# Kernel tuning notes

Measured on AMD Instinct MI355X. Metric: run time of the kernel, lower is better.

Reference implementation:

```python
import jax, jax.numpy as jnp
import numpy as np


def setup_inputs() -> dict:
    key = jax.random.key(0)
    k0, k1, k2 = jax.random.split(key, 3)
    B, S, H, D = 2, 2048, 16, 128  # flash-attn layout [batch, seq, heads, head_dim]
    q = jax.random.normal(k0, (B, S, H, D), dtype=jnp.float32)
    k = jax.random.normal(k1, (B, S, H, D), dtype=jnp.float32)
    v = jax.random.normal(k2, (B, S, H, D), dtype=jnp.float32)
    return {"_in0": q, "_in1": k, "_in2": v}


def reference(_in0, _in1, _in2):
    # Ring attention computes exact (non-causal, default) scaled dot-product
    # attention over the full sequence; the ring KV rotation is a distributed
    # execution detail, not a change in math. Single-device math:
    q, k, v = _in0, _in1, _in2
    D = q.shape[-1]
    scale = 1.0 / jnp.sqrt(jnp.asarray(D, dtype=q.dtype))
    # scores: [B, H, Sq, Sk]
    scores = jnp.einsum("bqhd,bkhd->bhqk", q, k) * scale
    probs = jax.nn.softmax(scores, axis=-1)
    out = jnp.einsum("bhqk,bkhd->bqhd", probs, v)
    return out
```

## Files before the change

kernel.cpp:

```cpp
#include <hip/hip_runtime.h>
#include <hip/hip_bf16.h>

typedef __attribute__((ext_vector_type(8))) short short8;
typedef __attribute__((ext_vector_type(16))) float f32x16;
typedef __attribute__((ext_vector_type(4))) unsigned int uint4v;

#define NB 2
#define NS 2048
#define NH 16
#define ND 128
#define ROWS (NH * ND)
#define KVBLK 64
#define QBLK 128
#define NTILE (NS / KVBLK)
#define NQB (NS / QBLK)
#define TILEB 16384

__device__ __forceinline__ unsigned short f2bf(float f) {
  union { __hip_bfloat16 b; unsigned short u; } c;
  c.b = __float2bfloat16(f);
  return c.u;
}

__device__ __forceinline__ short8 pack8(float4 a, float4 b, float s) {
  short8 r;
  r[0] = (short)f2bf(a.x * s); r[1] = (short)f2bf(a.y * s);
  r[2] = (short)f2bf(a.z * s); r[3] = (short)f2bf(a.w * s);
  r[4] = (short)f2bf(b.x * s); r[5] = (short)f2bf(b.y * s);
  r[6] = (short)f2bf(b.z * s); r[7] = (short)f2bf(b.w * s);
  return r;
}

__device__ __forceinline__ void dma16(const void* g, void* l) {
  __builtin_amdgcn_global_load_lds(
      (const __attribute__((address_space(1))) unsigned int*)g,
      (__attribute__((address_space(3))) unsigned int*)l, 16, 0, 0);
}

__device__ __forceinline__ void pl32swap(unsigned int& a, unsigned int& b) {
  asm("v_permlane32_swap_b32 %0, %1" : "+v"(a), "+v"(b));
}

__global__ __launch_bounds__(256) void prepass_kv(
    const float* __restrict__ Kg, const float* __restrict__ Vg,
    char* __restrict__ Kbt, char* __restrict__ Vbt) {
  const int blk = blockIdx.x;
  const int t = blk & (NTILE - 1);
  const int bh = blk >> 5;
  const int h = bh & (NH - 1);
  const int b = bh >> 4;
  const int tid = threadIdx.x;

  const size_t ibase = (size_t)b * NS * ROWS + (size_t)h * ND + (size_t)t * KVBLK * ROWS;
  const float* Kp = Kg + ibase;
  const float* Vp = Vg + ibase;
  char* Kt = Kbt + (size_t)blk * TILEB;
  char* Vt = Vbt + (size_t)blk * TILEB;

#pragma unroll
  for (int j = 0; j < 4; ++j) {
    const int r = j * 16 + (tid >> 4);
    const int c = tid & 15;
    const float* src = Kp + (size_t)r * ROWS + c * 8;
    float4 a = *reinterpret_cast<const float4*>(src);
    float4 d = *reinterpret_cast<const float4*>(src + 4);
    *reinterpret_cast<short8*>(Kt + r * 256 + (((c ^ (r & 15)) << 4))) = pack8(a, d, 1.0f);
  }

  __shared__ float vt[64][129];
#pragma unroll
  for (int j = 0; j < 4; ++j) {
    const int r = j * 16 + (tid >> 4);
    const int c0 = (tid & 15) * 8;
    float4 a = *reinterpret_cast<const float4*>(Vp + (size_t)r * ROWS + c0);
    float4 d = *reinterpret_cast<const float4*>(Vp + (size_t)r * ROWS + c0 + 4);
    vt[r][c0 + 0] = a.x; vt[r][c0 + 1] = a.y; vt[r][c0 + 2] = a.z; vt[r][c0 + 3] = a.w;
    vt[r][c0 + 4] = d.x; vt[r][c0 + 5] = d.y; vt[r][c0 + 6] = d.z; vt[r][c0 + 7] = d.w;
  }
  __syncthreads();
#pragma unroll
  for (int it = 0; it < 4; ++it) {
    const int item = it * 256 + tid;
    const int r = item >> 4;
    const int j = item & 15;
    const int d = 2 * r + (j >> 3);
    const int k0 = (j & 7) * 8;
    short8 o8;
#pragma unroll
    for (int i = 0; i < 8; ++i) o8[i] = (short)f2bf(vt[k0 + i][d]);
    *reinterpret_cast<short8*>(Vt + r * 256 + (((j ^ (r & 15)) << 4))) = o8;
  }
}

__global__ __launch_bounds__(256, 2) void fattn_fwd(
    const float* __restrict__ Qg, const char* __restrict__ Kbt,
    const char* __restrict__ Vbt, float* __restrict__ Og) {
  __shared__ __align__(16) char lds[65536];
  const int tid = threadIdx.x;
  const int l = tid & 63;
  const int w = tid >> 6;
  const int l31 = l & 31;
  const int hi2 = l >> 5;

  const int orig = blockIdx.x;
  const int wg = (orig & 7) * 64 + (orig >> 3);
  const int qblk = wg & (NQB - 1);
  const int bh = wg >> 4;
  const int h = bh & (NH - 1);
  const int b = bh >> 4;

  const float* Qp = Qg + (size_t)b * NS * ROWS + (size_t)h * ND;
  float* Op = Og + (size_t)b * NS * ROWS + (size_t)h * ND;
  const char* Ktiles = Kbt + (size_t)bh * NTILE * TILEB;
  const char* Vtiles = Vbt + (size_t)bh * NTILE * TILEB;

  const float scale = 0.08838834764831845f * 1.4426950408889634f;

  const int qrow = qblk * QBLK + w * 32 + l31;
  short8 qf[8];
  {
    const float* qr = Qp + (size_t)qrow * ROWS + hi2 * 8;
#pragma unroll
    for (int ks = 0; ks < 8; ++ks) {
      float4 a = *reinterpret_cast<const float4*>(qr + ks * 16);
      float4 c = *reinterpret_cast<const float4*>(qr + ks * 16 + 4);
      qf[ks] = pack8(a, c, scale);
    }
  }

  auto stage = [&](int t, char* kd, char* vd) {
    const char* Ksrc = Ktiles + (size_t)t * TILEB;
    const char* Vsrc = Vtiles + (size_t)t * TILEB;
#pragma unroll
    for (int i = 0; i < 4; ++i) {
      const int instr = w * 4 + i;
      dma16(Ksrc + instr * 1024 + l * 16, kd + instr * 1024);
    }
#pragma unroll
    for (int i = 0; i < 4; ++i) {
      const int instr = w * 4 + i;
      dma16(Vsrc + instr * 1024 + l * 16, vd + instr * 1024);
    }
  };

  f32x16 o[4];
#pragma unroll
  for (int dt = 0; dt < 4; ++dt) o[dt] = 0.f;
  float l_acc = 0.f;

  stage(0, lds, lds + 16384);
  asm volatile("s_waitcnt vmcnt(0)" ::: "memory");
  __syncthreads();

#pragma unroll 1
  for (int t = 0; t < NTILE; ++t) {
    char* ksb = lds + (t & 1) * 32768;
    char* vtb = ksb + 16384;
    if (t + 1 < NTILE) {
      char* kn = lds + ((t + 1) & 1) * 32768;
      stage(t + 1, kn, kn + 16384);
    }

    short8 pf[4];
#pragma unroll
    for (int mt = 0; mt < 2; ++mt) {
      f32x16 acc = 0.f;
      const int row = mt * 32 + l31;
      const int rsw = (row & 15) << 4;
      __builtin_amdgcn_s_setprio(1);
#pragma unroll
      for (int ks = 0; ks < 8; ++ks) {
        short8 kf = *reinterpret_cast<const short8*>(
            ksb + row * 256 + ((ks * 32 + hi2 * 16) ^ rsw));
        acc = __builtin_amdgcn_mfma_f32_32x32x16_bf16(kf, qf[ks], acc, 0, 0, 0);
      }
      __builtin_amdgcn_s_setprio(0);
      f32x16 p;
#pragma unroll
      for (int r = 0; r < 16; ++r) p[r] = exp2f(acc[r]);
      {
        float s = 0.f;
#pragma unroll
        for (int r = 0; r < 16; ++r) s += p[r];
        l_acc += s;
      }
#pragma unroll
      for (int half = 0; half < 2; ++half) {
        unsigned int X[4];
#pragma unroll
        for (int j = 0; j < 4; ++j)
          X[j] = (unsigned int)f2bf(p[half * 8 + 2 * j]) |
                 ((unsigned int)f2bf(p[half * 8 + 2 * j + 1]) << 16);
        pl32swap(X[0], X[2]);
        pl32swap(X[1], X[3]);
        uint4v u = {X[0], X[1], X[2], X[3]};
        pf[mt * 2 + half] = __builtin_bit_cast(short8, u);
      }
    }

    __builtin_amdgcn_s_setprio(1);
#pragma unroll
    for (int dt = 0; dt < 4; ++dt) {
      const int d = dt * 32 + l31;
      const int vrow = d >> 1;
      const int vsw = (vrow & 15) << 4;
      const int doff = (d & 1) * 128;
#pragma unroll
      for (int ks = 0; ks < 4; ++ks) {
        short8 vf = *reinterpret_cast<const short8*>(
            vtb + vrow * 256 + ((doff + ks * 32 + hi2 * 16) ^ vsw));
        o[dt] = __builtin_amdgcn_mfma_f32_32x32x16_bf16(vf, pf[ks], o[dt], 0, 0, 0);
      }
    }
    __builtin_amdgcn_s_setprio(0);

    if (t + 1 < NTILE) {
      asm volatile("s_waitcnt vmcnt(0)" ::: "memory");
      __syncthreads();
    }
  }

  const float lt = l_acc + __shfl_xor(l_acc, 32);
  const float inv = 1.0f / lt;
  float* orow = Op + (size_t)qrow * ROWS;
#pragma unroll
  for (int dt = 0; dt < 4; ++dt) {
#pragma unroll
    for (int g = 0; g < 4; ++g) {
      float4 v;
      v.x = o[dt][g * 4 + 0] * inv;
      v.y = o[dt][g * 4 + 1] * inv;
      v.z = o[dt][g * 4 + 2] * inv;
      v.w = o[dt][g * 4 + 3] * inv;
      *reinterpret_cast<float4*>(orow + dt * 32 + g * 8 + hi2 * 4) = v;
    }
  }
}

extern "C" void kernel_launch(void* const* d_in, const int* in_sizes, int n_in,
                              void* d_out, int out_size, void* d_ws, size_t ws_size,
                              hipStream_t stream) {
  const float* q = (const float*)d_in[0];
  const float* k = (const float*)d_in[1];
  const float* v = (const float*)d_in[2];
  float* out = (float*)d_out;
  (void)in_sizes; (void)n_in; (void)out_size; (void)ws_size;
  char* Kbt = (char*)d_ws;
  char* Vbt = Kbt + (size_t)NB * NH * NTILE * TILEB;
  prepass_kv<<<dim3(NB * NH * NTILE), dim3(256), 0, stream>>>(k, v, Kbt, Vbt);
  fattn_fwd<<<dim3(NQB * NB * NH), dim3(256), 0, stream>>>(q, Kbt, Vbt, out);
}
```

Before: 110.5 us.

## Double Q block per workgroup and process two KV tiles per sync window

Query block size grows from 128 to 256 rows with 512 threads (8 waves), so each staged K/V tile is reused by twice as many query rows. LDS doubles to 128KB to hold two KV tiles per double-buffered window, which halves the number of barriers. The QK step now interleaves four independent MFMA accumulators for more ILP, and per-lane LDS offsets are computed once up front. The risks are register pressure under the new launch bounds, which could cause spills, and only one workgroup fitting per CU.

```diff
diff --git a/kernel.cpp b/kernel.cpp
--- a/kernel.cpp
+++ b/kernel.cpp
@@ -11,9 +11,10 @@
 #define ND 128
 #define ROWS (NH * ND)
 #define KVBLK 64
-#define QBLK 128
+#define QBLK 256
 #define NTILE (NS / KVBLK)
 #define NQB (NS / QBLK)
+#define NWIN (NTILE / 2)
 #define TILEB 16384
 
 __device__ __forceinline__ unsigned short f2bf(float f) {
@@ -92,10 +93,10 @@
   }
 }
 
-__global__ __launch_bounds__(256, 2) void fattn_fwd(
+__global__ __launch_bounds__(512, 2) void fattn_fwd(
     const float* __restrict__ Qg, const char* __restrict__ Kbt,
     const char* __restrict__ Vbt, float* __restrict__ Og) {
-  __shared__ __align__(16) char lds[65536];
+  __shared__ __align__(16) char lds[131072];
   const int tid = threadIdx.x;
   const int l = tid & 63;
   const int w = tid >> 6;
@@ -103,9 +104,9 @@
   const int hi2 = l >> 5;
 
   const int orig = blockIdx.x;
-  const int wg = (orig & 7) * 64 + (orig >> 3);
+  const int wg = (orig & 7) * 32 + (orig >> 3);
   const int qblk = wg & (NQB - 1);
-  const int bh = wg >> 4;
+  const int bh = wg >> 3;
   const int h = bh & (NH - 1);
   const int b = bh >> 4;
 
@@ -128,18 +129,29 @@
     }
   }
 
-  auto stage = [&](int t, char* kd, char* vd) {
-    const char* Ksrc = Ktiles + (size_t)t * TILEB;
-    const char* Vsrc = Vtiles + (size_t)t * TILEB;
-#pragma unroll
-    for (int i = 0; i < 4; ++i) {
-      const int instr = w * 4 + i;
-      dma16(Ksrc + instr * 1024 + l * 16, kd + instr * 1024);
-    }
-#pragma unroll
-    for (int i = 0; i < 4; ++i) {
-      const int instr = w * 4 + i;
-      dma16(Vsrc + instr * 1024 + l * 16, vd + instr * 1024);
+  int qkoff[8], pvoff[4];
+  {
+    const int rsw = (l31 & 15) << 4;
+#pragma unroll
+    for (int ks = 0; ks < 8; ++ks)
+      qkoff[ks] = l31 * 256 + ((ks * 32 + hi2 * 16) ^ rsw);
+    const int vsw = ((l31 >> 1) & 15) << 4;
+#pragma unroll
+    for (int ks = 0; ks < 4; ++ks)
+      pvoff[ks] = (l31 >> 1) * 256 +
+                  ((((l31 & 1) * 128) + ks * 32 + hi2 * 16) ^ vsw);
+  }
+
+  auto stageT = [&](int t, int s) {
+    const char* Ks = Ktiles + (size_t)t * TILEB;
+    const char* Vs = Vtiles + (size_t)t * TILEB;
+    char* kd = lds + s * 32768;
+    char* vd = kd + 16384;
+#pragma unroll
+    for (int i = 0; i < 2; ++i) {
+      const int off = i * 8192 + w * 1024;
+      dma16(Ks + off + l * 16, kd + off);
+      dma16(Vs + off + l * 16, vd + off);
     }
   };
 
@@ -148,73 +160,80 @@
   for (int dt = 0; dt < 4; ++dt) o[dt] = 0.f;
   float l_acc = 0.f;
 
-  stage(0, lds, lds + 16384);
+  auto smpack = [&](const f32x16& acc, short8* out2) {
+    f32x16 p;
+#pragma unroll
+    for (int r = 0; r < 16; ++r) p[r] = exp2f(acc[r]);
+    float s = 0.f;
+#pragma unroll
+    for (int r = 0; r < 16; ++r) s += p[r];
+    l_acc += s;
+#pragma unroll
+    for (int half = 0; half < 2; ++half) {
+      unsigned int X[4];
+#pragma unroll
+      for (int j = 0; j < 4; ++j)
+        X[j] = (unsigned int)f2bf(p[half * 8 + 2 * j]) |
+               ((unsigned int)f2bf(p[half * 8 + 2 * j + 1]) << 16);
+      pl32swap(X[0], X[2]);
+      pl32swap(X[1], X[3]);
+      uint4v u = {X[0], X[1], X[2], X[3]};
+      out2[half] = __builtin_bit_cast(short8, u);
+    }
+  };
+
+  auto pv = [&](const char* vb, const short8* pf) {
+    __builtin_amdgcn_s_setprio(1);
+#pragma unroll
+    for (int dt = 0; dt < 4; ++dt) {
+#pragma unroll
+      for (int ks = 0; ks < 4; ++ks) {
+        short8 vf = *reinterpret_cast<const short8*>(vb + pvoff[ks] + dt * 4096);
+        o[dt] = __builtin_amdgcn_mfma_f32_32x32x16_bf16(vf, pf[ks], o[dt], 0, 0, 0);
+      }
+    }
+    __builtin_amdgcn_s_setprio(0);
+  };
+
+  stageT(0, 0);
+  stageT(1, 1);
   asm volatile("s_waitcnt vmcnt(0)" ::: "memory");
   __syncthreads();
 
 #pragma unroll 1
-  for (int t = 0; t < NTILE; ++t) {
-    char* ksb = lds + (t & 1) * 32768;
-    char* vtb = ksb + 16384;
-    if (t + 1 < NTILE) {
-      char* kn = lds + ((t + 1) & 1) * 32768;
-      stage(t + 1, kn, kn + 16384);
-    }
+  for (int j = 0; j < NWIN; ++j) {
+    if (j + 1 < NWIN) {
+      const int s0 = ((j & 1) ^ 1) * 2;
+      stageT(2 * j + 2, s0);
+      stageT(2 * j + 3, s0 + 1);
+    }
+    const char* kb0 = lds + (j & 1) * 65536;
+    const char* kb1 = kb0 + 32768;
+
+    f32x16 a00 = 0.f, a01 = 0.f, a10 = 0.f, a11 = 0.f;
+    __builtin_amdgcn_s_setprio(1);
+#pragma unroll
+    for (int ks = 0; ks < 8; ++ks) {
+      short8 k0 = *reinterpret_cast<const short8*>(kb0 + qkoff[ks]);
+      a00 = __builtin_amdgcn_mfma_f32_32x32x16_bf16(k0, qf[ks], a00, 0, 0, 0);
+      short8 k1 = *reinterpret_cast<const short8*>(kb0 + qkoff[ks] + 8192);
+      a01 = __builtin_amdgcn_mfma_f32_32x32x16_bf16(k1, qf[ks], a01, 0, 0, 0);
+      short8 k2 = *reinterpret_cast<const short8*>(kb1 + qkoff[ks]);
+      a10 = __builtin_amdgcn_mfma_f32_32x32x16_bf16(k2, qf[ks], a10, 0, 0, 0);
+      short8 k3 = *reinterpret_cast<const short8*>(kb1 + qkoff[ks] + 8192);
+      a11 = __builtin_amdgcn_mfma_f32_32x32x16_bf16(k3, qf[ks], a11, 0, 0, 0);
+    }
+    __builtin_amdgcn_s_setprio(0);
 
     short8 pf[4];
-#pragma unroll
-    for (int mt = 0; mt < 2; ++mt) {
-      f32x16 acc = 0.f;
-      const int row = mt * 32 + l31;
-      const int rsw = (row & 15) << 4;
-      __builtin_amdgcn_s_setprio(1);
-#pragma unroll
-      for (int ks = 0; ks < 8; ++ks) {
-        short8 kf = *reinterpret_cast<const short8*>(
-            ksb + row * 256 + ((ks * 32 + hi2 * 16) ^ rsw));
-        acc = __builtin_amdgcn_mfma_f32_32x32x16_bf16(kf, qf[ks], acc, 0, 0, 0);
-      }
-      __builtin_amdgcn_s_setprio(0);
-      f32x16 p;
-#pragma unroll
-      for (int r = 0; r < 16; ++r) p[r] = exp2f(acc[r]);
-      {
-        float s = 0.f;
-#pragma unroll
-        for (int r = 0; r < 16; ++r) s += p[r];
-        l_acc += s;
-      }
-#pragma unroll
-      for (int half = 0; half < 2; ++half) {
-        unsigned int X[4];
-#pragma unroll
-        for (int j = 0; j < 4; ++j)
-          X[j] = (unsigned int)f2bf(p[half * 8 + 2 * j]) |
-                 ((unsigned int)f2bf(p[half * 8 + 2 * j + 1]) << 16);
-        pl32swap(X[0], X[2]);
-        pl32swap(X[1], X[3]);
-        uint4v u = {X[0], X[1], X[2], X[3]};
-        pf[mt * 2 + half] = __builtin_bit_cast(short8, u);
-      }
-    }
-
-    __builtin_amdgcn_s_setprio(1);
-#pragma unroll
-    for (int dt = 0; dt < 4; ++dt) {
-      const int d = dt * 32 + l31;
-      const int vrow = d >> 1;
-      const int vsw = (vrow & 15) << 4;
-      const int doff = (d & 1) * 128;
-#pragma unroll
-      for (int ks = 0; ks < 4; ++ks) {
-        short8 vf = *reinterpret_cast<const short8*>(
-            vtb + vrow * 256 + ((doff + ks * 32 + hi2 * 16) ^ vsw));
-        o[dt] = __builtin_amdgcn_mfma_f32_32x32x16_bf16(vf, pf[ks], o[dt], 0, 0, 0);
-      }
-    }
-    __builtin_amdgcn_s_setprio(0);
-
-    if (t + 1 < NTILE) {
+    smpack(a00, pf + 0);
+    smpack(a01, pf + 2);
+    pv(kb0 + 16384, pf);
+    smpack(a10, pf + 0);
+    smpack(a11, pf + 2);
+    pv(kb1 + 16384, pf);
+
+    if (j + 1 < NWIN) {
       asm volatile("s_waitcnt vmcnt(0)" ::: "memory");
       __syncthreads();
     }
@@ -248,5 +267,5 @@
   char* Kbt = (char*)d_ws;
   char* Vbt = Kbt + (size_t)NB * NH * NTILE * TILEB;
   prepass_kv<<<dim3(NB * NH * NTILE), dim3(256), 0, stream>>>(k, v, Kbt, Vbt);
-  fattn_fwd<<<dim3(NQB * NB * NH), dim3(256), 0, stream>>>(q, Kbt, Vbt, out);
-}
+  fattn_fwd<<<dim3(NQB * NB * NH), dim3(512), 0, stream>>>(q, Kbt, Vbt, out);
+}
```

New measurement: 110.8 us. No clear change (+0.3%).

## Split KV across two workgroups, double Q rows per wave, add combine pass

Applied to the files above, without the earlier changes.

Each wave now handles 64 query rows, so every K/V fragment read from LDS feeds two MFMAs. The KV sequence is split in two halves processed by separate workgroups, which keeps the grid size unchanged. A separate combine kernel sums the partial outputs and normalizers. The prepass writes K/V directly in MFMA fragment order, so the swizzled address math goes away. The cost is extra global traffic for the fp32 partial outputs (two full-size buffers), a third kernel launch, and higher register pressure from 8 accumulators per wave.

```diff
diff --git a/kernel.cpp b/kernel.cpp
--- a/kernel.cpp
+++ b/kernel.cpp
@@ -11,10 +11,14 @@
 #define ND 128
 #define ROWS (NH * ND)
 #define KVBLK 64
-#define QBLK 128
 #define NTILE (NS / KVBLK)
+#define QBLK 256
 #define NQB (NS / QBLK)
+#define NSPLIT 2
+#define TPS (NTILE / NSPLIT)
 #define TILEB 16384
+#define ELEMS ((size_t)NB * NH * NS * ND)
+#define LCNT ((size_t)NB * NS * NH)
 
 __device__ __forceinline__ unsigned short f2bf(float f) {
   union { __hip_bfloat16 b; unsigned short u; } c;
@@ -43,58 +47,77 @@
 
 __global__ __launch_bounds__(256) void prepass_kv(
     const float* __restrict__ Kg, const float* __restrict__ Vg,
-    char* __restrict__ Kbt, char* __restrict__ Vbt) {
+    char* __restrict__ Kimg, char* __restrict__ Vimg) {
   const int blk = blockIdx.x;
   const int t = blk & (NTILE - 1);
   const int bh = blk >> 5;
   const int h = bh & (NH - 1);
   const int b = bh >> 4;
   const int tid = threadIdx.x;
+  const int l = tid & 63;
+  const int l31 = l & 31;
+  const int hi2 = l >> 5;
 
   const size_t ibase = (size_t)b * NS * ROWS + (size_t)h * ND + (size_t)t * KVBLK * ROWS;
   const float* Kp = Kg + ibase;
   const float* Vp = Vg + ibase;
-  char* Kt = Kbt + (size_t)blk * TILEB;
-  char* Vt = Vbt + (size_t)blk * TILEB;
+  char* Kt = Kimg + (size_t)blk * TILEB;
+  char* Vt = Vimg + (size_t)blk * TILEB;
+
+  __shared__ float st[64][129];
 
 #pragma unroll
   for (int j = 0; j < 4; ++j) {
     const int r = j * 16 + (tid >> 4);
-    const int c = tid & 15;
-    const float* src = Kp + (size_t)r * ROWS + c * 8;
-    float4 a = *reinterpret_cast<const float4*>(src);
-    float4 d = *reinterpret_cast<const float4*>(src + 4);
-    *reinterpret_cast<short8*>(Kt + r * 256 + (((c ^ (r & 15)) << 4))) = pack8(a, d, 1.0f);
-  }
-
-  __shared__ float vt[64][129];
+    const int c0 = (tid & 15) * 8;
+    float4 a = *reinterpret_cast<const float4*>(Kp + (size_t)r * ROWS + c0);
+    float4 d = *reinterpret_cast<const float4*>(Kp + (size_t)r * ROWS + c0 + 4);
+    st[r][c0 + 0] = a.x; st[r][c0 + 1] = a.y; st[r][c0 + 2] = a.z; st[r][c0 + 3] = a.w;
+    st[r][c0 + 4] = d.x; st[r][c0 + 5] = d.y; st[r][c0 + 6] = d.z; st[r][c0 + 7] = d.w;
+  }
+  __syncthreads();
+#pragma unroll
+  for (int it = 0; it < 4; ++it) {
+    const int item = it * 256 + tid;
+    const int g = item >> 6;
+    const int ll = item & 63;
+    const int row = (g >> 3) * 32 + (ll & 31);
+    const int kc = (g & 7) * 16 + (ll >> 5) * 8;
+    short8 o8;
+#pragma unroll
+    for (int e = 0; e < 8; ++e) o8[e] = (short)f2bf(st[row][kc + e]);
+    *reinterpret_cast<short8*>(Kt + (g * 64 + ll) * 16) = o8;
+  }
+  __syncthreads();
+
 #pragma unroll
   for (int j = 0; j < 4; ++j) {
     const int r = j * 16 + (tid >> 4);
     const int c0 = (tid & 15) * 8;
     float4 a = *reinterpret_cast<const float4*>(Vp + (size_t)r * ROWS + c0);
     float4 d = *reinterpret_cast<const float4*>(Vp + (size_t)r * ROWS + c0 + 4);
-    vt[r][c0 + 0] = a.x; vt[r][c0 + 1] = a.y; vt[r][c0 + 2] = a.z; vt[r][c0 + 3] = a.w;
-    vt[r][c0 + 4] = d.x; vt[r][c0 + 5] = d.y; vt[r][c0 + 6] = d.z; vt[r][c0 + 7] = d.w;
+    st[r][c0 + 0] = a.x; st[r][c0 + 1] = a.y; st[r][c0 + 2] = a.z; st[r][c0 + 3] = a.w;
+    st[r][c0 + 4] = d.x; st[r][c0 + 5] = d.y; st[r][c0 + 6] = d.z; st[r][c0 + 7] = d.w;
   }
   __syncthreads();
 #pragma unroll
   for (int it = 0; it < 4; ++it) {
     const int item = it * 256 + tid;
-    const int r = item >> 4;
-    const int j = item & 15;
-    const int d = 2 * r + (j >> 3);
-    const int k0 = (j & 7) * 8;
+    const int g = item >> 6;
+    const int ll = item & 63;
+    const int d = (g >> 2) * 32 + (ll & 31);
+    const int kv = (g & 3) * 16 + (ll >> 5) * 8;
     short8 o8;
 #pragma unroll
-    for (int i = 0; i < 8; ++i) o8[i] = (short)f2bf(vt[k0 + i][d]);
-    *reinterpret_cast<short8*>(Vt + r * 256 + (((j ^ (r & 15)) << 4))) = o8;
-  }
-}
-
-__global__ __launch_bounds__(256, 2) void fattn_fwd(
-    const float* __restrict__ Qg, const char* __restrict__ Kbt,
-    const char* __restrict__ Vbt, float* __restrict__ Og) {
+    for (int e = 0; e < 8; ++e) o8[e] = (short)f2bf(st[kv + e][d]);
+    *reinterpret_cast<short8*>(Vt + (g * 64 + ll) * 16) = o8;
+  }
+}
+
+__global__ __launch_bounds__(256, 2) void fattn_split(
+    const float* __restrict__ Qg, const char* __restrict__ Kimg,
+    const char* __restrict__ Vimg, float* __restrict__ Obase,
+    float* __restrict__ Lbase) {
   __shared__ __align__(16) char lds[65536];
   const int tid = threadIdx.x;
   const int l = tid & 63;
@@ -105,135 +128,165 @@
   const int orig = blockIdx.x;
   const int wg = (orig & 7) * 64 + (orig >> 3);
   const int qblk = wg & (NQB - 1);
+  const int split = (wg >> 3) & 1;
   const int bh = wg >> 4;
   const int h = bh & (NH - 1);
   const int b = bh >> 4;
 
+  float* Opart = Obase + (size_t)split * ELEMS;
+  float* Lpart = Lbase + (size_t)split * LCNT;
+
   const float* Qp = Qg + (size_t)b * NS * ROWS + (size_t)h * ND;
-  float* Op = Og + (size_t)b * NS * ROWS + (size_t)h * ND;
-  const char* Ktiles = Kbt + (size_t)bh * NTILE * TILEB;
-  const char* Vtiles = Vbt + (size_t)bh * NTILE * TILEB;
+  const char* Kt = Kimg + (size_t)bh * NTILE * TILEB;
+  const char* Vt = Vimg + (size_t)bh * NTILE * TILEB;
 
   const float scale = 0.08838834764831845f * 1.4426950408889634f;
 
-  const int qrow = qblk * QBLK + w * 32 + l31;
-  short8 qf[8];
+  const int qrow0 = qblk * QBLK + w * 64 + l31;
+  short8 qf0[8], qf1[8];
   {
-    const float* qr = Qp + (size_t)qrow * ROWS + hi2 * 8;
+    const float* qr0 = Qp + (size_t)qrow0 * ROWS + hi2 * 8;
+    const float* qr1 = qr0 + (size_t)32 * ROWS;
 #pragma unroll
     for (int ks = 0; ks < 8; ++ks) {
-      float4 a = *reinterpret_cast<const float4*>(qr + ks * 16);
-      float4 c = *reinterpret_cast<const float4*>(qr + ks * 16 + 4);
-      qf[ks] = pack8(a, c, scale);
-    }
-  }
-
-  auto stage = [&](int t, char* kd, char* vd) {
-    const char* Ksrc = Ktiles + (size_t)t * TILEB;
-    const char* Vsrc = Vtiles + (size_t)t * TILEB;
+      float4 a = *reinterpret_cast<const float4*>(qr0 + ks * 16);
+      float4 c = *reinterpret_cast<const float4*>(qr0 + ks * 16 + 4);
+      qf0[ks] = pack8(a, c, scale);
+      float4 d = *reinterpret_cast<const float4*>(qr1 + ks * 16);
+      float4 e = *reinterpret_cast<const float4*>(qr1 + ks * 16 + 4);
+      qf1[ks] = pack8(d, e, scale);
+    }
+  }
+
+  const int lo16 = l * 16;
+
+  auto stage = [&](int t, int slot) {
+    const char* Ks = Kt + (size_t)t * TILEB;
+    const char* Vs = Vt + (size_t)t * TILEB;
+    char* kd = lds + slot * 32768;
+    char* vd = kd + 16384;
 #pragma unroll
     for (int i = 0; i < 4; ++i) {
-      const int instr = w * 4 + i;
-      dma16(Ksrc + instr * 1024 + l * 16, kd + instr * 1024);
-    }
-#pragma unroll
-    for (int i = 0; i < 4; ++i) {
-      const int instr = w * 4 + i;
-      dma16(Vsrc + instr * 1024 + l * 16, vd + instr * 1024);
+      const int off = (w * 4 + i) * 1024;
+      dma16(Ks + off + lo16, kd + off);
+      dma16(Vs + off + lo16, vd + off);
     }
   };
 
-  f32x16 o[4];
-#pragma unroll
-  for (int dt = 0; dt < 4; ++dt) o[dt] = 0.f;
-  float l_acc = 0.f;
-
-  stage(0, lds, lds + 16384);
+  f32x16 o[4][2];
+#pragma unroll
+  for (int dt = 0; dt < 4; ++dt) {
+    o[dt][0] = 0.f;
+    o[dt][1] = 0.f;
+  }
+  float lac0 = 0.f, lac1 = 0.f;
+
+  auto sm = [&](const f32x16& acc, short8& f0, short8& f1, float& lac) {
+    f32x16 p;
+#pragma unroll
+    for (int r = 0; r < 16; ++r) p[r] = exp2f(acc[r]);
+    float s01 = (p[0] + p[1]) + (p[2] + p[3]);
+    float s23 = (p[4] + p[5]) + (p[6] + p[7]);
+    float s45 = (p[8] + p[9]) + (p[10] + p[11]);
+    float s67 = (p[12] + p[13]) + (p[14] + p[15]);
+    lac += (s01 + s23) + (s45 + s67);
+    unsigned int X[4];
+#pragma unroll
+    for (int j = 0; j < 4; ++j)
+      X[j] = (unsigned int)f2bf(p[2 * j]) | ((unsigned int)f2bf(p[2 * j + 1]) << 16);
+    pl32swap(X[0], X[2]);
+    pl32swap(X[1], X[3]);
+    uint4v u0 = {X[0], X[1], X[2], X[3]};
+    f0 = __builtin_bit_cast(short8, u0);
+    unsigned int Y[4];
+#pragma unroll
+    for (int j = 0; j < 4; ++j)
+      Y[j] = (unsigned int)f2bf(p[8 + 2 * j]) | ((unsigned int)f2bf(p[8 + 2 * j + 1]) << 16);
+    pl32swap(Y[0], Y[2]);
+    pl32swap(Y[1], Y[3]);
+    uint4v u1 = {Y[0], Y[1], Y[2], Y[3]};
+    f1 = __builtin_bit_cast(short8, u1);
+  };
+
+  stage(split * TPS, 0);
   asm volatile("s_waitcnt vmcnt(0)" ::: "memory");
   __syncthreads();
 
 #pragma unroll 1
-  for (int t = 0; t < NTILE; ++t) {
-    char* ksb = lds + (t & 1) * 32768;
-    char* vtb = ksb + 16384;
-    if (t + 1 < NTILE) {
-      char* kn = lds + ((t + 1) & 1) * 32768;
-      stage(t + 1, kn, kn + 16384);
-    }
-
-    short8 pf[4];
+  for (int tt = 0; tt < TPS; ++tt) {
+    const int t = split * TPS + tt;
+    if (tt + 1 < TPS) stage(t + 1, (tt + 1) & 1);
+    const char* kb = lds + (tt & 1) * 32768;
+    const char* vb = kb + 16384;
+
 #pragma unroll
     for (int mt = 0; mt < 2; ++mt) {
-      f32x16 acc = 0.f;
-      const int row = mt * 32 + l31;
-      const int rsw = (row & 15) << 4;
-      __builtin_amdgcn_s_setprio(1);
+      f32x16 a0 = 0.f, a1 = 0.f;
 #pragma unroll
       for (int ks = 0; ks < 8; ++ks) {
-        short8 kf = *reinterpret_cast<const short8*>(
-            ksb + row * 256 + ((ks * 32 + hi2 * 16) ^ rsw));
-        acc = __builtin_amdgcn_mfma_f32_32x32x16_bf16(kf, qf[ks], acc, 0, 0, 0);
+        short8 kf = *reinterpret_cast<const short8*>(kb + lo16 + (mt * 8 + ks) * 1024);
+        a0 = __builtin_amdgcn_mfma_f32_32x32x16_bf16(kf, qf0[ks], a0, 0, 0, 0);
+        a1 = __builtin_amdgcn_mfma_f32_32x32x16_bf16(kf, qf1[ks], a1, 0, 0, 0);
       }
-      __builtin_amdgcn_s_setprio(0);
-      f32x16 p;
-#pragma unroll
-      for (int r = 0; r < 16; ++r) p[r] = exp2f(acc[r]);
-      {
-        float s = 0.f;
-#pragma unroll
-        for (int r = 0; r < 16; ++r) s += p[r];
-        l_acc += s;
+      short8 f00, f01, f10, f11;
+      sm(a0, f00, f01, lac0);
+      sm(a1, f10, f11, lac1);
+#pragma unroll
+      for (int dt = 0; dt < 4; ++dt) {
+        short8 v0 = *reinterpret_cast<const short8*>(vb + lo16 + (dt * 4 + mt * 2) * 1024);
+        o[dt][0] = __builtin_amdgcn_mfma_f32_32x32x16_bf16(v0, f00, o[dt][0], 0, 0, 0);
+        o[dt][1] = __builtin_amdgcn_mfma_f32_32x32x16_bf16(v0, f10, o[dt][1], 0, 0, 0);
+        short8 v1 = *reinterpret_cast<const short8*>(vb + lo16 + (dt * 4 + mt * 2 + 1) * 1024);
+        o[dt][0] = __builtin_amdgcn_mfma_f32_32x32x16_bf16(v1, f01, o[dt][0], 0, 0, 0);
+        o[dt][1] = __builtin_amdgcn_mfma_f32_32x32x16_bf16(v1, f11, o[dt][1], 0, 0, 0);
       }
-#pragma unroll
-      for (int half = 0; half < 2; ++half) {
-        unsigned int X[4];
-#pragma unroll
-        for (int j = 0; j < 4; ++j)
-          X[j] = (unsigned int)f2bf(p[half * 8 + 2 * j]) |
-                 ((unsigned int)f2bf(p[half * 8 + 2 * j + 1]) << 16);
-        pl32swap(X[0], X[2]);
-        pl32swap(X[1], X[3]);
-        uint4v u = {X[0], X[1], X[2], X[3]};
-        pf[mt * 2 + half] = __builtin_bit_cast(short8, u);
-      }
-    }
-
-    __builtin_amdgcn_s_setprio(1);
-#pragma unroll
-    for (int dt = 0; dt < 4; ++dt) {
-      const int d = dt * 32 + l31;
-      const int vrow = d >> 1;
-      const int vsw = (vrow & 15) << 4;
-      const int doff = (d & 1) * 128;
-#pragma unroll
-      for (int ks = 0; ks < 4; ++ks) {
-        short8 vf = *reinterpret_cast<const short8*>(
-            vtb + vrow * 256 + ((doff + ks * 32 + hi2 * 16) ^ vsw));
-        o[dt] = __builtin_amdgcn_mfma_f32_32x32x16_bf16(vf, pf[ks], o[dt], 0, 0, 0);
-      }
-    }
-    __builtin_amdgcn_s_setprio(0);
-
-    if (t + 1 < NTILE) {
+    }
+
+    if (tt + 1 < TPS) {
       asm volatile("s_waitcnt vmcnt(0)" ::: "memory");
       __syncthreads();
     }
   }
 
-  const float lt = l_acc + __shfl_xor(l_acc, 32);
-  const float inv = 1.0f / lt;
-  float* orow = Op + (size_t)qrow * ROWS;
-#pragma unroll
-  for (int dt = 0; dt < 4; ++dt) {
-#pragma unroll
-    for (int g = 0; g < 4; ++g) {
-      float4 v;
-      v.x = o[dt][g * 4 + 0] * inv;
-      v.y = o[dt][g * 4 + 1] * inv;
-      v.z = o[dt][g * 4 + 2] * inv;
-      v.w = o[dt][g * 4 + 3] * inv;
-      *reinterpret_cast<float4*>(orow + dt * 32 + g * 8 + hi2 * 4) = v;
-    }
+  const float lt0 = lac0 + __shfl_xor(lac0, 32);
+  const float lt1 = lac1 + __shfl_xor(lac1, 32);
+#pragma unroll
+  for (int qh = 0; qh < 2; ++qh) {
+    const int qr = qrow0 + qh * 32;
+    float* orow = Opart + ((size_t)(b * NS + qr) * NH + h) * ND;
+#pragma unroll
+    for (int dt = 0; dt < 4; ++dt) {
+#pragma unroll
+      for (int g = 0; g < 4; ++g) {
+        float4 v;
+        v.x = o[dt][qh][g * 4 + 0];
+        v.y = o[dt][qh][g * 4 + 1];
+        v.z = o[dt][qh][g * 4 + 2];
+        v.w = o[dt][qh][g * 4 + 3];
+        *reinterpret_cast<float4*>(orow + dt * 32 + g * 8 + hi2 * 4) = v;
+      }
+    }
+    if (hi2 == 0) Lpart[(size_t)(b * NS + qr) * NH + h] = qh ? lt1 : lt0;
+  }
+}
+
+__global__ __launch_bounds__(256) void combine_splits(
+    const float4* __restrict__ O0, const float4* __restrict__ O1,
+    const float* __restrict__ L0, const float* __restrict__ L1,
+    float4* __restrict__ out, int nf4) {
+  int i = blockIdx.x * 256 + threadIdx.x;
+  const int stride = gridDim.x * 256;
+  for (; i < nf4; i += stride) {
+    const int r = i >> 5;
+    float4 a = O0[i];
+    float4 c = O1[i];
+    const float inv = 1.0f / (L0[r] + L1[r]);
+    float4 v;
+    v.x = (a.x + c.x) * inv;
+    v.y = (a.y + c.y) * inv;
+    v.z = (a.z + c.z) * inv;
+    v.w = (a.w + c.w) * inv;
+    out[i] = v;
   }
 }
 
@@ -245,8 +298,14 @@
   const float* v = (const float*)d_in[2];
   float* out = (float*)d_out;
   (void)in_sizes; (void)n_in; (void)out_size; (void)ws_size;
-  char* Kbt = (char*)d_ws;
-  char* Vbt = Kbt + (size_t)NB * NH * NTILE * TILEB;
-  prepass_kv<<<dim3(NB * NH * NTILE), dim3(256), 0, stream>>>(k, v, Kbt, Vbt);
-  fattn_fwd<<<dim3(NQB * NB * NH), dim3(256), 0, stream>>>(q, Kbt, Vbt, out);
-}
+  char* Kimg = (char*)d_ws;
+  char* Vimg = Kimg + (size_t)NB * NH * NTILE * TILEB;
+  float* Obase = (float*)d_ws + ELEMS;
+  float* Lbase = Obase + 2 * ELEMS;
+  prepass_kv<<<dim3(NB * NH * NTILE), dim3(256), 0, stream>>>(k, v, Kimg, Vimg);
+  fattn_split<<<dim3(NSPLIT * NQB * NB * NH), dim3(256), 0, stream>>>(
+      q, Kimg, Vimg, Obase, Lbase);
+  combine_splits<<<dim3(2048), dim3(256), 0, stream>>>(
+      (const float4*)Obase, (const float4*)(Obase + ELEMS), Lbase, Lbase + LCNT,
+      (float4*)out, (int)(ELEMS / 4));
+}
```

Result: slower. 198.2 us (+79.3%).
